# Performance work log

Hardware: AMD Instinct MI355X
Metric: run time of the kernel (lower is better)

The kernel has to match this reference:

```python
import jax, jax.numpy as jnp
import numpy as np

NEG_SLOPE = 0.01  # F.leaky_relu default
N_NODES = 50000
N_EDGES = 800000
DIMS = [1, 64, 128, 64, 1]


def _lrelu(x):
    return jnp.where(x >= 0, x, NEG_SLOPE * x)


def _gconv(x, src, dst, W, b, n):
    # DGL GraphConv, norm='none': sum-aggregate src features into dst, then linear.
    # (DGL multiplies first when in_feats > out_feats; identical math since sum is linear.)
    if x.shape[1] > W.shape[1]:
        x = x @ W
        return jax.ops.segment_sum(x[src], dst, num_segments=n) + b
    agg = jax.ops.segment_sum(x[src], dst, num_segments=n)  # [n, d_in]
    return agg @ W + b


def setup_inputs() -> dict:
    key = jax.random.key(0)
    ks = jax.random.split(key, 16)
    inp = {
        "in_feat": jax.random.normal(ks[0], (N_NODES, 1), jnp.float32),
        "src": jax.random.randint(ks[1], (N_EDGES,), 0, N_NODES),
        "dst": jax.random.randint(ks[2], (N_EDGES,), 0, N_NODES),
    }
    for i in range(4):
        fi, fo = DIMS[i], DIMS[i + 1]
        scale = (2.0 / (fi + fo)) ** 0.5  # xavier-style
        inp[f"W{i}"] = jax.random.normal(ks[3 + 2 * i], (fi, fo), jnp.float32) * scale
        inp[f"b{i}"] = jax.random.normal(ks[4 + 2 * i], (fo,), jnp.float32) * 0.01
    return inp


def reference(in_feat, src, dst, W0, b0, W1, b1, W2, b2, W3, b3):
    n = in_feat.shape[0]
    h = _lrelu(_gconv(in_feat, src, dst, W0, b0, n))
    h = _lrelu(_gconv(h, src, dst, W1, b1, n))
    h = _lrelu(_gconv(h, src, dst, W2, b2, n))
    h = _lrelu(_gconv(h, src, dst, W3, b3, n))
    return h[1]  # node index 1, shape (1,)
```

## Files before the change

### kernel.cpp

```cpp
#include <hip/hip_runtime.h>

#define N_NODES 50000
#define N_EDGES 800000
#define NE4 (N_EDGES / 4)
#define NMASKW 1568
#define C1MAX 64
#define CAP   16
#define S2MAX 1024
#define DMAX  4096
#define BK    96
#define SB1   ((NE4 + 255) / 256)
#define G34   512
#define FGRID 256
#define SUBW  64

#define AS(p, v)  __hip_atomic_store((p), (v), __ATOMIC_RELAXED, __HIP_MEMORY_SCOPE_AGENT)
#define ALD(p)    __hip_atomic_load((p), __ATOMIC_RELAXED, __HIP_MEMORY_SCOPE_AGENT)
#define AADD(p,v) __hip_atomic_fetch_add((p), (v), __ATOMIC_RELAXED, __HIP_MEMORY_SCOPE_AGENT)

__device__ __forceinline__ float lrelu(float v) { return v >= 0.f ? v : 0.01f * v; }
__device__ __forceinline__ bool mtest(const unsigned int* m, int i) {
    return (m[i >> 5] >> (i & 31)) & 1u;
}

__global__ __launch_bounds__(256) void scan1_k(const int4* __restrict__ dst4,
                                               const int* __restrict__ src,
                                               int* __restrict__ e1cnt, int* __restrict__ e1val,
                                               unsigned int* __restrict__ zbase, int zwords) {
    __shared__ int lcnt;
    __shared__ int lval[CAP];
    const int tid = threadIdx.x;
    const int t = blockIdx.x * 256 + tid;
    if (tid == 0) lcnt = 0;
    __syncthreads();
    if (t < zwords) zbase[t] = 0u;
    if (t < NE4) {
        int4 d4 = dst4[t];
        int dv[4] = { d4.x, d4.y, d4.z, d4.w };
#pragma unroll
        for (int k = 0; k < 4; ++k) {
            if (dv[k] == 1) {
                int q = atomicAdd(&lcnt, 1);
                if (q < CAP) lval[q] = src[t * 4 + k];
            }
        }
    }
    __syncthreads();
    int c = lcnt < CAP ? lcnt : CAP;
    if (tid == 0) e1cnt[blockIdx.x] = c;
    if (tid < c) e1val[blockIdx.x * CAP + tid] = lval[tid];
}

__global__ __launch_bounds__(256) void scan2_k(const int4* __restrict__ dst4,
                                               const int* __restrict__ src,
                                               const int* __restrict__ e1cnt,
                                               const int* __restrict__ e1val,
                                               unsigned int* __restrict__ f2m,
                                               int* __restrict__ pos2, int* __restrict__ cnt2,
                                               int2* __restrict__ eD, int* __restrict__ cntD,
                                               int* __restrict__ mult, int* __restrict__ cnt1g) {
    __shared__ unsigned int msk[NMASKW];
    __shared__ int candN[C1MAX];
    __shared__ int candC;
    const int tid = threadIdx.x;
    for (int k = tid; k < NMASKW; k += 256) msk[k] = 0u;
    if (tid == 0) candC = 0;
    __syncthreads();
    for (int b = tid; b < SB1; b += 256) {
        int c = e1cnt[b]; if (c > CAP) c = CAP;
        for (int i = 0; i < c; ++i) {
            int n = e1val[b * CAP + i];
            unsigned int bit = 1u << (n & 31);
            unsigned int old = atomicOr(&msk[n >> 5], bit);
            if (!(old & bit)) { int q = atomicAdd(&candC, 1); if (q < C1MAX) candN[q] = n; }
        }
    }
    __syncthreads();
    int c1 = candC; if (c1 > C1MAX) c1 = C1MAX;
    if (blockIdx.x == 0 && tid == 0) AS(cnt1g, c1);
    int t = blockIdx.x * 256 + tid;
    if (t >= NE4) return;
    int4 d4 = dst4[t];
    int dv[4] = { d4.x, d4.y, d4.z, d4.w };
#pragma unroll
    for (int k = 0; k < 4; ++k) {
        int dd = dv[k];
        if (dd == 1) {
            int ss = src[t * 4 + k];
            int r = 0;
            for (int u = 0; u < c1; ++u) r += (candN[u] < ss);
            atomicAdd(&mult[r], 1);
        }
        if (mtest(msk, dd)) {
            int ss = src[t * 4 + k];
            unsigned int bit = 1u << (ss & 31);
            unsigned int old = atomicOr(&f2m[ss >> 5], bit);
            if (!(old & bit)) {
                int q2 = atomicAdd(cnt2, 1);
                if (q2 < S2MAX) AS(&pos2[ss], q2);
            }
            int r = 0;
            for (int u = 0; u < c1; ++u) r += (candN[u] < dd);
            int q = atomicAdd(cntD, 1);
            if (q < DMAX) {
                unsigned long long ev = (unsigned long long)(unsigned int)ss |
                                        ((unsigned long long)(unsigned int)r << 32);
                AS((unsigned long long*)&eD[q], ev);
            }
        }
    }
}

__global__ __launch_bounds__(256) void scan34_k(const int4* __restrict__ dst4,
                                                const int* __restrict__ src,
                                                const int4* __restrict__ src4,
                                                const float* __restrict__ x,
                                                const unsigned int* __restrict__ f2m,
                                                unsigned int* __restrict__ f3m,
                                                const int* __restrict__ pos2,
                                                float* __restrict__ agg0,
                                                int* __restrict__ bucket,
                                                int* __restrict__ slotCnt,
                                                const int2* __restrict__ eD,
                                                const int* __restrict__ cntD,
                                                int2* __restrict__ eDr,
                                                int* __restrict__ sub, int* __restrict__ top,
                                                int* __restrict__ rel) {
    __shared__ unsigned int msk[NMASKW];
    const int tid = threadIdx.x;
    const int gid = blockIdx.x * 256 + tid;
    const int T = G34 * 256;

    for (int k = tid; k < NMASKW; k += 256) msk[k] = f2m[k];
    __syncthreads();
    for (int t = gid; t < NE4; t += T) {
        int4 d4 = dst4[t];
        int dv[4] = { d4.x, d4.y, d4.z, d4.w };
#pragma unroll
        for (int k = 0; k < 4; ++k) {
            int dd = dv[k];
            if (mtest(msk, dd)) {
                int ss = src[t * 4 + k];
                unsigned int bit = 1u << (ss & 31);
                unsigned int old = atomicOr(&f3m[ss >> 5], bit);
                if (!(old & bit)) AS(&agg0[ss], 0.f);
                int sl = pos2[dd];
                if ((unsigned)sl < S2MAX) {
                    int bi = atomicAdd(&slotCnt[sl], 1);
                    if (bi < BK) AS(&bucket[sl * BK + bi], ss);
                }
            }
        }
    }
    __syncthreads();
    if (tid == 0) {
        int s = blockIdx.x & 7;
        int old = AADD(&sub[s * SUBW], 1);
        if (old == (G34 / 8) - 1) {
            int o2 = AADD(top, 1);
            if (o2 == 7) AS(rel, 1);
        }
        while (ALD(rel) == 0) __builtin_amdgcn_s_sleep(8);
    }
    __syncthreads();

    {
        int cD = *cntD; if (cD > DMAX) cD = DMAX;
        if (gid < cD) {
            int2 e = eD[gid];
            int sl = pos2[e.x];
            unsigned long long ev =
                (unsigned long long)(unsigned int)((unsigned)sl < S2MAX ? sl : -1) |
                ((unsigned long long)(unsigned int)e.y << 32);
            AS((unsigned long long*)&eDr[gid], ev);
        }
    }
    for (int k = tid; k < NMASKW; k += 256) msk[k] = f3m[k];
    __syncthreads();
    for (int t = gid; t < NE4; t += T) {
        int4 d4 = dst4[t];
        bool m0 = mtest(msk, d4.x), m1 = mtest(msk, d4.y);
        bool m2 = mtest(msk, d4.z), m3 = mtest(msk, d4.w);
        if (m0 | m1 | m2 | m3) {
            int4 s4 = src4[t];
            if (m0) atomicAdd(&agg0[d4.x], x[s4.x]);
            if (m1) atomicAdd(&agg0[d4.y], x[s4.y]);
            if (m2) atomicAdd(&agg0[d4.z], x[s4.z]);
            if (m3) atomicAdd(&agg0[d4.w], x[s4.w]);
        }
    }
}

struct PS {
    const int* bucket; const int* slotCnt; const float* agg0;
    const float* W0; const float* b0; const float* W1; const float* b1; const float* W2;
    const float* b2; const float* W3; const float* b3;
    const int* cnt2; const int2* eDr; const int* cntD;
    const int* mult; const int* cnt1g;
    float* gacc; int* subD; int* topD; float* out;
};

__global__ __launch_bounds__(256) void slots_k(PS p) {
    __shared__ float xv[128];
    __shared__ float part[256];
    __shared__ float rowA[64];
    __shared__ float rowH[128];
    __shared__ float rowT[64];
    __shared__ float t3s[C1MAX];
    __shared__ int lflag;
    const int tid = threadIdx.x;
    const int g = tid >> 6, j = tid & 63;
    int c2 = *p.cnt2;
    int cD = *p.cntD;
    int myCnt0 = p.slotCnt[blockIdx.x];
    int bidx0 = (tid < BK) ? p.bucket[blockIdx.x * BK + tid] : 0;
    int2 e0 = (tid < DMAX) ? p.eDr[tid] : make_int2(-1, -1);
    if (c2 > S2MAX) c2 = S2MAX;
    if (cD > DMAX) cD = DMAX;
    const float w0 = p.W0[j], bb0 = p.b0[j];

    for (int b = blockIdx.x; b < c2; b += FGRID) {
        int cnt = (b == (int)blockIdx.x) ? myCnt0 : p.slotCnt[b];
        if (cnt > BK) cnt = BK;
        int bidx = (b == (int)blockIdx.x) ? bidx0
                 : ((tid < BK) ? p.bucket[b * BK + tid] : 0);
        if (tid < cnt) xv[tid] = p.agg0[bidx];
        __syncthreads();
        float racc = 0.f;
        for (int m = g; m < cnt; m += 4) racc += lrelu(xv[m] * w0 + bb0);
        part[tid] = racc;
        __syncthreads();
        if (tid < 64)
            rowA[tid] = part[tid] + part[64 + tid] + part[128 + tid] + part[192 + tid];
        __syncthreads();
        if (tid < 128) {
            float h = p.b1[tid];
#pragma unroll
            for (int k = 0; k < 64; ++k) h += rowA[k] * p.W1[k * 128 + tid];
            rowH[tid] = lrelu(h);
        }
        __syncthreads();
        if (tid < 64) {
            float a2 = 0.f;
#pragma unroll
            for (int k = 0; k < 128; ++k) a2 += rowH[k] * p.W2[k * 64 + tid];
            rowT[tid] = a2;
        }
        __syncthreads();
        for (int base = 0; base < cD; base += 256) {
            int i = base + tid;
            int2 e = (base == 0) ? e0 : make_int2(-1, -1);
            if (base != 0 && i < cD) e = p.eDr[i];
            bool m = (e.x == b) && (i < cD);
            unsigned long long bal = __ballot(m);
            while (bal) {
                int bit = __builtin_ctzll(bal); bal &= bal - 1;
                int sl1 = __shfl(e.y, bit, 64);
                if ((unsigned)sl1 < C1MAX)
                    atomicAdd(&p.gacc[sl1 * 64 + j], rowT[j]);
            }
        }
        __syncthreads();
    }

    __syncthreads();
    if (tid == 0) {
        lflag = 0;
        int s = blockIdx.x & 7;
        int old = AADD(&p.subD[s * SUBW], 1);
        if (old == (FGRID / 8) - 1) {
            int o2 = AADD(p.topD, 1);
            lflag = (o2 == 7);
        }
    }
    __syncthreads();
    if (!lflag) return;

    {
        int c1 = *p.cnt1g; if (c1 > C1MAX) c1 = C1MAX;
        int w = tid >> 6;
        for (int r = w; r < c1; r += 4) {
            float v = lrelu(p.gacc[r * 64 + j] + p.b2[j]) * p.W3[j];
            for (int off = 32; off > 0; off >>= 1) v += __shfl_down(v, off, 64);
            if (j == 0) t3s[r] = v;
        }
        __syncthreads();
        if (tid == 0) {
            float s = 0.f;
            for (int r = 0; r < c1; ++r) s += (float)p.mult[r] * t3s[r];
            p.out[0] = lrelu(s + p.b3[0]);
        }
    }
}

extern "C" void kernel_launch(void* const* d_in, const int* in_sizes, int n_in,
                              void* d_out, int out_size, void* d_ws, size_t ws_size,
                              hipStream_t stream) {
    const float* x   = (const float*)d_in[0];
    const int*   src = (const int*)d_in[1];
    const int*   dst = (const int*)d_in[2];
    const float* W0 = (const float*)d_in[3];  const float* b0 = (const float*)d_in[4];
    const float* W1 = (const float*)d_in[5];  const float* b1 = (const float*)d_in[6];
    const float* W2 = (const float*)d_in[7];  const float* b2 = (const float*)d_in[8];
    const float* W3 = (const float*)d_in[9];  const float* b3 = (const float*)d_in[10];
    float* out = (float*)d_out;
    const int4* dst4 = (const int4*)dst;
    const int4* src4 = (const int4*)src;

    char* base = (char*)d_ws;
    size_t off = 0;
    auto take = [&](size_t bytes) { char* q = base + off; off += (bytes + 255) & ~(size_t)255; return q; };
    unsigned int* f2m = (unsigned int*)take(NMASKW * 4);
    unsigned int* f3m = (unsigned int*)take(NMASKW * 4);
    int* cnt2  = (int*)take(4);
    int* cntD  = (int*)take(4);
    int* cnt1g = (int*)take(4);
    int* mult  = (int*)take((size_t)C1MAX * 4);
    int* sub   = (int*)take((size_t)8 * SUBW * 4);
    int* top   = (int*)take(4);
    int* rel   = (int*)take(4);
    int* subD  = (int*)take((size_t)8 * SUBW * 4);
    int* topD  = (int*)take(4);
    int* slotCnt = (int*)take((size_t)S2MAX * 4);
    float* gacc  = (float*)take((size_t)C1MAX * 64 * 4);
    int zwords = (int)(off / 4);
    float* agg0   = (float*)take((size_t)N_NODES * 4);
    int*   e1cnt  = (int*)take((size_t)SB1 * 4);
    int*   e1val  = (int*)take((size_t)SB1 * CAP * 4);
    int2*  eD     = (int2*)take((size_t)DMAX * 8);
    int2*  eDr    = (int2*)take((size_t)DMAX * 8);
    int*   bucket = (int*)take((size_t)S2MAX * BK * 4);
    int*   pos2   = (int*)take((size_t)N_NODES * 4);

    scan1_k<<<SB1, 256, 0, stream>>>(dst4, src, e1cnt, e1val, (unsigned int*)base, zwords);
    scan2_k<<<SB1, 256, 0, stream>>>(dst4, src, e1cnt, e1val, f2m, pos2, cnt2, eD, cntD,
                                     mult, cnt1g);
    scan34_k<<<G34, 256, 0, stream>>>(dst4, src, src4, x, f2m, f3m, pos2, agg0,
                                      bucket, slotCnt, eD, cntD, eDr, sub, top, rel);

    PS hp;
    hp.bucket = bucket; hp.slotCnt = slotCnt; hp.agg0 = agg0;
    hp.W0 = W0; hp.b0 = b0; hp.W1 = W1; hp.b1 = b1; hp.W2 = W2;
    hp.b2 = b2; hp.W3 = W3; hp.b3 = b3;
    hp.cnt2 = cnt2; hp.eDr = eDr; hp.cntD = cntD;
    hp.mult = mult; hp.cnt1g = cnt1g;
    hp.gacc = gacc; hp.subD = subD; hp.topD = topD; hp.out = out;
    slots_k<<<FGRID, 256, 0, stream>>>(hp);
}
```

Before: 129.7 us.

## Fuse scan2 and scan34 into one persistent kernel with phased grid barriers

Merges the second edge scan into the persistent scan34 kernel, so one 512-block launch walks the edges with a grid-stride loop and separates the phases with a reusable multi-phase grid barrier. The barrier writes its release flag to eight padded slots, one per sub-counter group, so waiting blocks poll different cache lines. This removes one kernel launch and its inter-kernel gap. In exchange, each block now has to rebuild the candidate mask from e1cnt/e1val, the scan2 work runs on fewer threads, and the barrier assumes all 512 blocks are resident at once.

```diff
diff --git a/kernel.cpp b/kernel.cpp
--- a/kernel.cpp
+++ b/kernel.cpp
@@ -10,7 +10,7 @@
 #define DMAX  4096
 #define BK    96
 #define SB1   ((NE4 + 255) / 256)
-#define G34   512
+#define GMEGA 512
 #define FGRID 256
 #define SUBW  64
 
@@ -21,6 +21,23 @@
 __device__ __forceinline__ float lrelu(float v) { return v >= 0.f ? v : 0.01f * v; }
 __device__ __forceinline__ bool mtest(const unsigned int* m, int i) {
     return (m[i >> 5] >> (i & 31)) & 1u;
+}
+
+__device__ __forceinline__ void gsyncM(int* sub, int* top, int* relArr, int ph) {
+    __syncthreads();
+    if (threadIdx.x == 0) {
+        int s = blockIdx.x & 7;
+        int old = AADD(&sub[s * SUBW], 1);
+        if (old == ph * (GMEGA / 8) - 1) {
+            int o2 = AADD(top, 1);
+            if (o2 == ph * 8 - 1) {
+#pragma unroll
+                for (int i = 0; i < 8; ++i) AS(&relArr[i * SUBW], ph);
+            }
+        }
+        while (ALD(&relArr[s * SUBW]) < ph) __builtin_amdgcn_s_sleep(16);
+    }
+    __syncthreads();
 }
 
 __global__ __launch_bounds__(256) void scan1_k(const int4* __restrict__ dst4,
@@ -51,25 +68,30 @@
     if (tid < c) e1val[blockIdx.x * CAP + tid] = lval[tid];
 }
 
-__global__ __launch_bounds__(256) void scan2_k(const int4* __restrict__ dst4,
-                                               const int* __restrict__ src,
-                                               const int* __restrict__ e1cnt,
-                                               const int* __restrict__ e1val,
-                                               unsigned int* __restrict__ f2m,
-                                               int* __restrict__ pos2, int* __restrict__ cnt2,
-                                               int2* __restrict__ eD, int* __restrict__ cntD,
-                                               int* __restrict__ mult, int* __restrict__ cnt1g) {
+struct PM {
+    const int4* dst4; const int* src; const int4* src4; const float* x;
+    const int* e1cnt; const int* e1val;
+    unsigned int* f2m; unsigned int* f3m;
+    int* pos2; int* cnt2; int2* eD; int* cntD; int* mult; int* cnt1g;
+    float* agg0; int* bucket; int* slotCnt; int2* eDr;
+    int* sub; int* top; int* relArr;
+};
+
+__global__ __launch_bounds__(256) void mega_k(PM p) {
     __shared__ unsigned int msk[NMASKW];
     __shared__ int candN[C1MAX];
     __shared__ int candC;
     const int tid = threadIdx.x;
+    const int gid = blockIdx.x * 256 + tid;
+    const int T = GMEGA * 256;
+
     for (int k = tid; k < NMASKW; k += 256) msk[k] = 0u;
     if (tid == 0) candC = 0;
     __syncthreads();
     for (int b = tid; b < SB1; b += 256) {
-        int c = e1cnt[b]; if (c > CAP) c = CAP;
+        int c = p.e1cnt[b]; if (c > CAP) c = CAP;
         for (int i = 0; i < c; ++i) {
-            int n = e1val[b * CAP + i];
+            int n = p.e1val[b * CAP + i];
             unsigned int bit = 1u << (n & 31);
             unsigned int old = atomicOr(&msk[n >> 5], bit);
             if (!(old & bit)) { int q = atomicAdd(&candC, 1); if (q < C1MAX) candN[q] = n; }
@@ -77,116 +99,86 @@
     }
     __syncthreads();
     int c1 = candC; if (c1 > C1MAX) c1 = C1MAX;
-    if (blockIdx.x == 0 && tid == 0) AS(cnt1g, c1);
-    int t = blockIdx.x * 256 + tid;
-    if (t >= NE4) return;
-    int4 d4 = dst4[t];
-    int dv[4] = { d4.x, d4.y, d4.z, d4.w };
-#pragma unroll
-    for (int k = 0; k < 4; ++k) {
-        int dd = dv[k];
-        if (dd == 1) {
-            int ss = src[t * 4 + k];
-            int r = 0;
-            for (int u = 0; u < c1; ++u) r += (candN[u] < ss);
-            atomicAdd(&mult[r], 1);
-        }
-        if (mtest(msk, dd)) {
-            int ss = src[t * 4 + k];
-            unsigned int bit = 1u << (ss & 31);
-            unsigned int old = atomicOr(&f2m[ss >> 5], bit);
-            if (!(old & bit)) {
-                int q2 = atomicAdd(cnt2, 1);
-                if (q2 < S2MAX) AS(&pos2[ss], q2);
-            }
-            int r = 0;
-            for (int u = 0; u < c1; ++u) r += (candN[u] < dd);
-            int q = atomicAdd(cntD, 1);
-            if (q < DMAX) {
-                unsigned long long ev = (unsigned long long)(unsigned int)ss |
-                                        ((unsigned long long)(unsigned int)r << 32);
-                AS((unsigned long long*)&eD[q], ev);
-            }
-        }
-    }
-}
-
-__global__ __launch_bounds__(256) void scan34_k(const int4* __restrict__ dst4,
-                                                const int* __restrict__ src,
-                                                const int4* __restrict__ src4,
-                                                const float* __restrict__ x,
-                                                const unsigned int* __restrict__ f2m,
-                                                unsigned int* __restrict__ f3m,
-                                                const int* __restrict__ pos2,
-                                                float* __restrict__ agg0,
-                                                int* __restrict__ bucket,
-                                                int* __restrict__ slotCnt,
-                                                const int2* __restrict__ eD,
-                                                const int* __restrict__ cntD,
-                                                int2* __restrict__ eDr,
-                                                int* __restrict__ sub, int* __restrict__ top,
-                                                int* __restrict__ rel) {
-    __shared__ unsigned int msk[NMASKW];
-    const int tid = threadIdx.x;
-    const int gid = blockIdx.x * 256 + tid;
-    const int T = G34 * 256;
-
-    for (int k = tid; k < NMASKW; k += 256) msk[k] = f2m[k];
-    __syncthreads();
+    if (blockIdx.x == 0 && tid == 0) AS(p.cnt1g, c1);
     for (int t = gid; t < NE4; t += T) {
-        int4 d4 = dst4[t];
+        int4 d4 = p.dst4[t];
+        int dv[4] = { d4.x, d4.y, d4.z, d4.w };
+#pragma unroll
+        for (int k = 0; k < 4; ++k) {
+            int dd = dv[k];
+            if (dd == 1) {
+                int ss = p.src[t * 4 + k];
+                int r = 0;
+                for (int u = 0; u < c1; ++u) r += (candN[u] < ss);
+                atomicAdd(&p.mult[r], 1);
+            }
+            if (mtest(msk, dd)) {
+                int ss = p.src[t * 4 + k];
+                unsigned int bit = 1u << (ss & 31);
+                unsigned int old = atomicOr(&p.f2m[ss >> 5], bit);
+                if (!(old & bit)) {
+                    int q2 = atomicAdd(p.cnt2, 1);
+                    if (q2 < S2MAX) AS(&p.pos2[ss], q2);
+                }
+                int r = 0;
+                for (int u = 0; u < c1; ++u) r += (candN[u] < dd);
+                int q = atomicAdd(p.cntD, 1);
+                if (q < DMAX) {
+                    unsigned long long ev = (unsigned long long)(unsigned int)ss |
+                                            ((unsigned long long)(unsigned int)r << 32);
+                    AS((unsigned long long*)&p.eD[q], ev);
+                }
+            }
+        }
+    }
+    gsyncM(p.sub, p.top, p.relArr, 1);
+
+    for (int k = tid; k < NMASKW; k += 256) msk[k] = p.f2m[k];
+    __syncthreads();
+    for (int t = gid; t < NE4; t += T) {
+        int4 d4 = p.dst4[t];
         int dv[4] = { d4.x, d4.y, d4.z, d4.w };
 #pragma unroll
         for (int k = 0; k < 4; ++k) {
             int dd = dv[k];
             if (mtest(msk, dd)) {
-                int ss = src[t * 4 + k];
+                int ss = p.src[t * 4 + k];
                 unsigned int bit = 1u << (ss & 31);
-                unsigned int old = atomicOr(&f3m[ss >> 5], bit);
-                if (!(old & bit)) AS(&agg0[ss], 0.f);
-                int sl = pos2[dd];
+                unsigned int old = atomicOr(&p.f3m[ss >> 5], bit);
+                if (!(old & bit)) AS(&p.agg0[ss], 0.f);
+                int sl = p.pos2[dd];
                 if ((unsigned)sl < S2MAX) {
-                    int bi = atomicAdd(&slotCnt[sl], 1);
-                    if (bi < BK) AS(&bucket[sl * BK + bi], ss);
+                    int bi = atomicAdd(&p.slotCnt[sl], 1);
+                    if (bi < BK) AS(&p.bucket[sl * BK + bi], ss);
                 }
             }
         }
     }
-    __syncthreads();
-    if (tid == 0) {
-        int s = blockIdx.x & 7;
-        int old = AADD(&sub[s * SUBW], 1);
-        if (old == (G34 / 8) - 1) {
-            int o2 = AADD(top, 1);
-            if (o2 == 7) AS(rel, 1);
-        }
-        while (ALD(rel) == 0) __builtin_amdgcn_s_sleep(8);
-    }
-    __syncthreads();
+    gsyncM(p.sub, p.top, p.relArr, 2);
 
     {
-        int cD = *cntD; if (cD > DMAX) cD = DMAX;
+        int cD = *p.cntD; if (cD > DMAX) cD = DMAX;
         if (gid < cD) {
-            int2 e = eD[gid];
-            int sl = pos2[e.x];
+            int2 e = p.eD[gid];
+            int sl = p.pos2[e.x];
             unsigned long long ev =
                 (unsigned long long)(unsigned int)((unsigned)sl < S2MAX ? sl : -1) |
                 ((unsigned long long)(unsigned int)e.y << 32);
-            AS((unsigned long long*)&eDr[gid], ev);
-        }
-    }
-    for (int k = tid; k < NMASKW; k += 256) msk[k] = f3m[k];
+            AS((unsigned long long*)&p.eDr[gid], ev);
+        }
+    }
+    for (int k = tid; k < NMASKW; k += 256) msk[k] = p.f3m[k];
     __syncthreads();
     for (int t = gid; t < NE4; t += T) {
-        int4 d4 = dst4[t];
+        int4 d4 = p.dst4[t];
         bool m0 = mtest(msk, d4.x), m1 = mtest(msk, d4.y);
         bool m2 = mtest(msk, d4.z), m3 = mtest(msk, d4.w);
         if (m0 | m1 | m2 | m3) {
-            int4 s4 = src4[t];
-            if (m0) atomicAdd(&agg0[d4.x], x[s4.x]);
-            if (m1) atomicAdd(&agg0[d4.y], x[s4.y]);
-            if (m2) atomicAdd(&agg0[d4.z], x[s4.z]);
-            if (m3) atomicAdd(&agg0[d4.w], x[s4.w]);
+            int4 s4 = p.src4[t];
+            if (m0) atomicAdd(&p.agg0[d4.x], p.x[s4.x]);
+            if (m1) atomicAdd(&p.agg0[d4.y], p.x[s4.y]);
+            if (m2) atomicAdd(&p.agg0[d4.z], p.x[s4.z]);
+            if (m3) atomicAdd(&p.agg0[d4.w], p.x[s4.w]);
         }
     }
 }
@@ -214,7 +206,7 @@
     int cD = *p.cntD;
     int myCnt0 = p.slotCnt[blockIdx.x];
     int bidx0 = (tid < BK) ? p.bucket[blockIdx.x * BK + tid] : 0;
-    int2 e0 = (tid < DMAX) ? p.eDr[tid] : make_int2(-1, -1);
+    int2 e0 = p.eDr[tid];
     if (c2 > S2MAX) c2 = S2MAX;
     if (cD > DMAX) cD = DMAX;
     const float w0 = p.W0[j], bb0 = p.b0[j];
@@ -318,7 +310,7 @@
     int* mult  = (int*)take((size_t)C1MAX * 4);
     int* sub   = (int*)take((size_t)8 * SUBW * 4);
     int* top   = (int*)take(4);
-    int* rel   = (int*)take(4);
+    int* relArr= (int*)take((size_t)8 * SUBW * 4);
     int* subD  = (int*)take((size_t)8 * SUBW * 4);
     int* topD  = (int*)take(4);
     int* slotCnt = (int*)take((size_t)S2MAX * 4);
@@ -333,10 +325,16 @@
     int*   pos2   = (int*)take((size_t)N_NODES * 4);
 
     scan1_k<<<SB1, 256, 0, stream>>>(dst4, src, e1cnt, e1val, (unsigned int*)base, zwords);
-    scan2_k<<<SB1, 256, 0, stream>>>(dst4, src, e1cnt, e1val, f2m, pos2, cnt2, eD, cntD,
-                                     mult, cnt1g);
-    scan34_k<<<G34, 256, 0, stream>>>(dst4, src, src4, x, f2m, f3m, pos2, agg0,
-                                      bucket, slotCnt, eD, cntD, eDr, sub, top, rel);
+
+    PM pm;
+    pm.dst4 = dst4; pm.src = src; pm.src4 = src4; pm.x = x;
+    pm.e1cnt = e1cnt; pm.e1val = e1val;
+    pm.f2m = f2m; pm.f3m = f3m;
+    pm.pos2 = pos2; pm.cnt2 = cnt2; pm.eD = eD; pm.cntD = cntD;
+    pm.mult = mult; pm.cnt1g = cnt1g;
+    pm.agg0 = agg0; pm.bucket = bucket; pm.slotCnt = slotCnt; pm.eDr = eDr;
+    pm.sub = sub; pm.top = top; pm.relArr = relArr;
+    mega_k<<<GMEGA, 256, 0, stream>>>(pm);
 
     PS hp;
     hp.bucket = bucket; hp.slotCnt = slotCnt; hp.agg0 = agg0;
```

After: 130.4 us. About the same (+0.6%).
